# Kernel tuning notes

Measured on AMD Instinct MI355X. Metric: run time of the kernel, lower is better.

## Reference

```python
import jax, jax.numpy as jnp
import numpy as np

B, S, D = 2, 2048, 1024
N_HEADS = 16
HEAD_DIM = D // N_HEADS  # 64, even for RoPE
THETA = 10000.0


def rope_tables(seq, head_dim, dtype=jnp.float32):
    half = head_dim // 2
    freqs = 1.0 / (THETA ** (jnp.arange(half, dtype=jnp.float32) / half))
    angles = jnp.arange(seq, dtype=jnp.float32)[:, None] * freqs[None, :]  # [S, half]
    return jnp.cos(angles).astype(dtype), jnp.sin(angles).astype(dtype)


def apply_rope_interleaved(x, cos, sin):
    # x: [b, h, s, d]; even/odd interleaving
    x_even = x[..., 0::2]
    x_odd = x[..., 1::2]
    r_even = x_even * cos - x_odd * sin
    r_odd = x_even * sin + x_odd * cos
    # interleave back: stack on last axis then reshape
    out = jnp.stack([r_even, r_odd], axis=-1).reshape(x.shape)
    return out


def setup_inputs() -> dict:
    key = jax.random.key(0)
    ks = jax.random.split(key, 6)
    scale = 1.0 / np.sqrt(D)
    return {
        "x": jax.random.normal(ks[0], (B, S, D), dtype=jnp.float32),
        "Wq": jax.random.normal(ks[1], (D, D), dtype=jnp.float32) * scale,
        "Wk": jax.random.normal(ks[2], (D, D), dtype=jnp.float32) * scale,
        "Wv": jax.random.normal(ks[3], (D, D), dtype=jnp.float32) * scale,
        "Wo": jax.random.normal(ks[4], (D, D), dtype=jnp.float32) * scale,
        "bo": jnp.zeros((D,), dtype=jnp.float32),
    }


def reference(x, Wq, Wk, Wv, Wo, bo):
    b, s, _ = x.shape
    # QKV projections (no bias), split heads -> [b, h, s, hd]
    def proj(W):
        return jnp.einsum('bsd,de->bse', x, W).reshape(b, s, N_HEADS, HEAD_DIM).transpose(0, 2, 1, 3)
    q, k, v = proj(Wq), proj(Wk), proj(Wv)

    cos, sin = rope_tables(s, HEAD_DIM, x.dtype)  # [s, hd//2]
    q = apply_rope_interleaved(q, cos, sin)
    k = apply_rope_interleaved(k, cos, sin)

    scale = 1.0 / jnp.sqrt(jnp.asarray(HEAD_DIM, dtype=x.dtype))
    scores = jnp.einsum('bhqd,bhkd->bhqk', q, k) * scale  # [b, h, s, s]
    causal = jnp.tril(jnp.ones((s, s), dtype=bool))
    scores = jnp.where(causal[None, None], scores, jnp.asarray(-jnp.inf, dtype=scores.dtype))
    attn = jax.nn.softmax(scores, axis=-1)
    ctx = jnp.einsum('bhqk,bhkd->bhqd', attn, v)  # [b, h, s, hd]
    ctx = ctx.transpose(0, 2, 1, 3).reshape(b, s, N_HEADS * HEAD_DIM)
    return jnp.einsum('bsd,de->bse', ctx, Wo) + bo
```

## Files before the change

### kernel.cpp

```cpp
#include <hip/hip_runtime.h>
#include <hip/hip_bf16.h>
#include <math.h>

constexpr int Bb   = 2;
constexpr int S    = 2048;
constexpr int D    = 1024;
constexpr int H    = 16;
constexpr int Dh   = 64;
constexpr int HALF = 32;
constexpr int M    = Bb * S;
constexpr int K    = 1024;
constexpr int N    = 1024;

typedef __attribute__((ext_vector_type(8))) short short8;
typedef __attribute__((ext_vector_type(4))) float f32x4;

__device__ __forceinline__ unsigned short f2bf(float f) {
    unsigned int u = __float_as_uint(f);
    unsigned int r = (u + 0x7fffu + ((u >> 16) & 1u)) >> 16;
    return (unsigned short)r;
}

__device__ __forceinline__ void gl_lds16(const unsigned short* g, unsigned short* lds_base) {
    __builtin_amdgcn_global_load_lds(
        (const __attribute__((address_space(1))) unsigned int*)g,
        (__attribute__((address_space(3))) unsigned int*)lds_base, 16, 0, 0);
}

__global__ __launch_bounds__(256) void prep_kernel(
    const float* __restrict__ x,
    const float* W0, const float* W1, const float* W2, const float* W3,
    unsigned short* __restrict__ xb,
    unsigned short* T0, unsigned short* T1, unsigned short* T2, unsigned short* T3,
    float* __restrict__ cosT, float* __restrict__ sinT)
{
    __shared__ float tile[64][65];
    const int bid = blockIdx.x;
    const int tid = threadIdx.x;

    if (bid < 256) {
        int idx = bid * 256 + tid;
        int s = idx >> 5;
        int i = idx & 31;
        double freq = exp(-(double)i * (log(10000.0) / 32.0));
        double ang  = (double)s * freq;
        cosT[idx] = (float)cos(ang);
        sinT[idx] = (float)sin(ang);
    } else if (bid < 256 + 4096) {
        size_t i = (size_t)(bid - 256) * 256 + tid;
        float4 v = *(const float4*)(x + i * 4);
        ushort4 pk;
        pk.x = f2bf(v.x); pk.y = f2bf(v.y); pk.z = f2bf(v.z); pk.w = f2bf(v.w);
        *(ushort4*)(xb + i * 4) = pk;
    } else {
        int wb = bid - 4352;
        int z  = wb >> 8;
        int rem = wb & 255;
        const float* W = (z == 0) ? W0 : (z == 1) ? W1 : (z == 2) ? W2 : W3;
        unsigned short* T = (z == 0) ? T0 : (z == 1) ? T1 : (z == 2) ? T2 : T3;
        const int bk = (rem >> 4) * 64;
        const int bn = (rem & 15) * 64;
        const int lr = tid >> 4;
        const int lc = (tid & 15) * 4;

        #pragma unroll
        for (int i = 0; i < 4; ++i) {
            int r = lr + i * 16;
            float4 v = *(const float4*)(W + (size_t)(bk + r) * N + bn + lc);
            tile[r][lc + 0] = v.x; tile[r][lc + 1] = v.y;
            tile[r][lc + 2] = v.z; tile[r][lc + 3] = v.w;
        }
        __syncthreads();
        #pragma unroll
        for (int i = 0; i < 4; ++i) {
            int nr = lr + i * 16;
            ushort4 pk;
            pk.x = f2bf(tile[lc + 0][nr]);
            pk.y = f2bf(tile[lc + 1][nr]);
            pk.z = f2bf(tile[lc + 2][nr]);
            pk.w = f2bf(tile[lc + 3][nr]);
            *(ushort4*)(T + (size_t)(bn + nr) * K + bk + lc) = pk;
        }
    }
}

__global__ __launch_bounds__(512, 2) void gemm_qkv_kernel(
    const unsigned short* __restrict__ A,
    const unsigned short* __restrict__ BT,
    unsigned short* outQ, unsigned short* outK, unsigned short* outV,
    const float* __restrict__ cosT, const float* __restrict__ sinT)
{
    constexpr int NT   = 32;
    constexpr int BUFS = 256 * 32;
    __shared__ __align__(16) unsigned short As[4 * BUFS];
    __shared__ __align__(16) unsigned short Bs[4 * BUFS];

    const int tid  = threadIdx.x;
    const int wid  = tid >> 6;
    const int lane = tid & 63;
    const int col  = lane & 15;
    const int quad = lane >> 4;
    const int wr   = wid >> 2;
    const int wc   = wid & 3;

    const int mbase = blockIdx.y * 256;
    const int nbase = blockIdx.x * 256;

    const int srow = lane >> 2;
    const int sch  = lane & 3;
    const unsigned short *pA0, *pA1, *pB0, *pB1;
    unsigned short *dA0, *dA1, *dB0, *dB1;
    {
        int r0 = wid * 16 + srow;
        int r1 = 128 + wid * 16 + srow;
        pA0 = A  + (size_t)(mbase + r0) * K + ((sch + (r0 >> 1)) & 3) * 8;
        pA1 = A  + (size_t)(mbase + r1) * K + ((sch + (r1 >> 1)) & 3) * 8;
        pB0 = BT + (size_t)(nbase + r0) * K + ((sch + (r0 >> 1)) & 3) * 8;
        pB1 = BT + (size_t)(nbase + r1) * K + ((sch + (r1 >> 1)) & 3) * 8;
        dA0 = &As[(wid * 16) * 32];
        dA1 = &As[(128 + wid * 16) * 32];
        dB0 = &Bs[(wid * 16) * 32];
        dB1 = &Bs[(128 + wid * 16) * 32];
    }

    int aoff[8], boff[4];
    #pragma unroll
    for (int f = 0; f < 8; ++f) {
        int r = wr * 128 + f * 16 + col;
        aoff[f] = r * 32 + ((quad - (r >> 1)) & 3) * 8;
    }
    #pragma unroll
    for (int n = 0; n < 4; ++n) {
        int r = wc * 64 + n * 16 + col;
        boff[n] = r * 32 + ((quad - (r >> 1)) & 3) * 8;
    }

    f32x4 acc[8][4];
    #pragma unroll
    for (int f = 0; f < 8; ++f)
        #pragma unroll
        for (int n = 0; n < 4; ++n) acc[f][n] = (f32x4)0.f;

    auto stageA = [&](int slot) {
        gl_lds16(pA0, dA0 + slot * BUFS); pA0 += 32;
        gl_lds16(pA1, dA1 + slot * BUFS); pA1 += 32;
    };
    auto stageB = [&](int slot) {
        gl_lds16(pB0, dB0 + slot * BUFS); pB0 += 32;
        gl_lds16(pB1, dB1 + slot * BUFS); pB1 += 32;
    };

    stageA(0); stageB(0);
    stageA(1); stageB(1);
    stageA(2); stageB(2);
    asm volatile("s_waitcnt vmcnt(8)" ::: "memory");
    __builtin_amdgcn_s_barrier();
    __builtin_amdgcn_sched_barrier(0);

    #pragma unroll 1
    for (int t = 0; t < NT; ++t) {
        const unsigned short* Ab = &As[(t & 3) * BUFS];
        const unsigned short* Bc = &Bs[(t & 3) * BUFS];
        const int nslot = (t + 3) & 3;
        short8 af[4], bf[4];

        #pragma unroll
        for (int i = 0; i < 4; ++i) af[i] = *(const short8*)&Ab[aoff[i]];
        #pragma unroll
        for (int n = 0; n < 4; ++n) bf[n] = *(const short8*)&Bc[boff[n]];
        if (t < NT - 3) stageA(nslot);
        __builtin_amdgcn_sched_barrier(0);
        __builtin_amdgcn_s_barrier();
        asm volatile("s_waitcnt lgkmcnt(0)" ::: "memory");
        __builtin_amdgcn_s_setprio(1);
        #pragma unroll
        for (int i = 0; i < 4; ++i)
            #pragma unroll
            for (int n = 0; n < 4; ++n)
                acc[i][n] = __builtin_amdgcn_mfma_f32_16x16x32_bf16(af[i], bf[n], acc[i][n], 0, 0, 0);
        __builtin_amdgcn_s_setprio(0);
        __builtin_amdgcn_sched_barrier(0);
        __builtin_amdgcn_s_barrier();
        __builtin_amdgcn_sched_barrier(0);

        #pragma unroll
        for (int i = 0; i < 4; ++i) af[i] = *(const short8*)&Ab[aoff[4 + i]];
        if (t < NT - 3) stageB(nslot);
        __builtin_amdgcn_sched_barrier(0);
        __builtin_amdgcn_s_barrier();
        asm volatile("s_waitcnt lgkmcnt(0)" ::: "memory");
        __builtin_amdgcn_s_setprio(1);
        #pragma unroll
        for (int i = 0; i < 4; ++i)
            #pragma unroll
            for (int n = 0; n < 4; ++n)
                acc[4 + i][n] = __builtin_amdgcn_mfma_f32_16x16x32_bf16(af[i], bf[n], acc[4 + i][n], 0, 0, 0);
        __builtin_amdgcn_s_setprio(0);
        if (t < NT - 3)       { asm volatile("s_waitcnt vmcnt(8)" ::: "memory"); }
        else if (t == NT - 3) { asm volatile("s_waitcnt vmcnt(4)" ::: "memory"); }
        else if (t == NT - 2) { asm volatile("s_waitcnt vmcnt(0)" ::: "memory"); }
        __builtin_amdgcn_s_barrier();
        __builtin_amdgcn_sched_barrier(0);
    }

    const int z = nbase >> 10;
    if (z < 2) {
        unsigned short* o = z ? outK : outQ;
        #pragma unroll
        for (int n = 0; n < 4; ++n) {
            int nl = (nbase & 1023) + wc * 64 + n * 16 + col;
            int h = nl >> 6, dh0 = nl & 63, p = dh0 >> 1;
            bool even = !(dh0 & 1);
            #pragma unroll
            for (int f = 0; f < 8; ++f)
                #pragma unroll
                for (int reg = 0; reg < 4; ++reg) {
                    int m_g = mbase + wr * 128 + f * 16 + quad * 4 + reg;
                    int b = m_g >> 11, s = m_g & 2047;
                    float v = acc[f][n][reg];
                    float part = __shfl_xor(v, 1, 64);
                    float c = cosT[s * HALF + p], sn = sinT[s * HALF + p];
                    float r = even ? (v * c - part * sn) : (v * c + part * sn);
                    o[((size_t)(b * H + h) * S + s) * Dh + dh0] = f2bf(r);
                }
        }
    } else {
        #pragma unroll
        for (int n = 0; n < 4; ++n) {
            int nl = (nbase & 1023) + wc * 64 + n * 16 + col;
            int h = nl >> 6, dh0 = nl & 63;
            #pragma unroll
            for (int f = 0; f < 8; ++f) {
                int m0 = mbase + wr * 128 + f * 16 + quad * 4;
                int b = m0 >> 11, s = m0 & 2047;
                ushort4 pk;
                pk.x = f2bf(acc[f][n][0]);
                pk.y = f2bf(acc[f][n][1]);
                pk.z = f2bf(acc[f][n][2]);
                pk.w = f2bf(acc[f][n][3]);
                *(ushort4*)&outV[((size_t)(b * H + h) * Dh + dh0) * S + s] = pk;
            }
        }
    }
}

__global__ __launch_bounds__(256) void gemm_out_kernel(
    const unsigned short* __restrict__ A,
    const unsigned short* __restrict__ BT,
    float* __restrict__ outO, const float* __restrict__ bias)
{
    constexpr int BK   = 64;
    constexpr int ABUF = 64 * BK;
    constexpr int BBUF = 64 * BK;
    __shared__ __align__(16) unsigned short As[2 * ABUF];
    __shared__ __align__(16) unsigned short Bs[2 * BBUF];

    const int tid  = threadIdx.x;
    const int wave = tid >> 6;
    const int lane = tid & 63;
    const int col  = lane & 15;
    const int quad = lane >> 4;
    const int wy   = wave >> 1;
    const int wx   = wave & 1;

    const int mbase = blockIdx.y * 64;
    const int nbase = blockIdx.x * 64;

    const int srow8 = lane >> 3;
    const int sch8  = lane & 7;

    const unsigned short *pA[2], *pB[2];
    unsigned short *dA[2], *dB[2];
    #pragma unroll
    for (int w = 0; w < 2; ++w) {
        int base = wave * 16 + w * 8;
        int tr = base + srow8;
        pA[w] = A  + (size_t)(mbase + tr) * K + ((sch8 + (tr >> 1)) & 7) * 8;
        pB[w] = BT + (size_t)(nbase + tr) * K + ((sch8 + (tr >> 1)) & 7) * 8;
        dA[w] = &As[base * BK];
        dB[w] = &Bs[base * BK];
    }

    int aoff[2][2], boff[2][2];
    #pragma unroll
    for (int ks = 0; ks < 2; ++ks) {
        #pragma unroll
        for (int mi = 0; mi < 2; ++mi) {
            int r = wy * 32 + mi * 16 + col;
            aoff[ks][mi] = r * BK + (((ks * 4 + quad) - (r >> 1)) & 7) * 8;
        }
        #pragma unroll
        for (int ni = 0; ni < 2; ++ni) {
            int r = wx * 32 + ni * 16 + col;
            boff[ks][ni] = r * BK + (((ks * 4 + quad) - (r >> 1)) & 7) * 8;
        }
    }

    f32x4 acc[2][2];
    #pragma unroll
    for (int mi = 0; mi < 2; ++mi)
        #pragma unroll
        for (int ni = 0; ni < 2; ++ni) acc[mi][ni] = (f32x4)0.f;

    auto stage = [&](int buf) {
        #pragma unroll
        for (int w = 0; w < 2; ++w) { gl_lds16(pA[w], dA[w] + buf * ABUF); pA[w] += BK; }
        #pragma unroll
        for (int w = 0; w < 2; ++w) { gl_lds16(pB[w], dB[w] + buf * BBUF); pB[w] += BK; }
    };
    auto compute = [&](int buf) {
        const unsigned short* Ac = &As[buf * ABUF];
        const unsigned short* Bc = &Bs[buf * BBUF];
        #pragma unroll
        for (int ks = 0; ks < 2; ++ks) {
            short8 af[2], bfr[2];
            #pragma unroll
            for (int mi = 0; mi < 2; ++mi) af[mi] = *(const short8*)&Ac[aoff[ks][mi]];
            #pragma unroll
            for (int ni = 0; ni < 2; ++ni) bfr[ni] = *(const short8*)&Bc[boff[ks][ni]];
            #pragma unroll
            for (int mi = 0; mi < 2; ++mi)
                #pragma unroll
                for (int ni = 0; ni < 2; ++ni)
                    acc[mi][ni] = __builtin_amdgcn_mfma_f32_16x16x32_bf16(af[mi], bfr[ni], acc[mi][ni], 0, 0, 0);
        }
    };

    stage(0);
    #pragma unroll 1
    for (int kk = 0; kk < 16; kk += 2) {
        __syncthreads();
        if (kk + 1 < 16) stage(1);
        compute(0);
        __syncthreads();
        if (kk + 2 < 16) stage(0);
        compute(1);
    }

    #pragma unroll
    for (int ni = 0; ni < 2; ++ni) {
        int n_g = nbase + wx * 32 + ni * 16 + col;
        float bv = bias[n_g];
        #pragma unroll
        for (int mi = 0; mi < 2; ++mi)
            #pragma unroll
            for (int reg = 0; reg < 4; ++reg) {
                int m_g = mbase + wy * 32 + mi * 16 + quad * 4 + reg;
                outO[(size_t)m_g * N + n_g] = acc[mi][ni][reg] + bv;
            }
    }
}

__global__ __launch_bounds__(256) void attn_mfma_kernel(
    const unsigned short* __restrict__ q, const unsigned short* __restrict__ k,
    const unsigned short* __restrict__ vt, unsigned short* __restrict__ ctx)
{
    constexpr int TSZ = 64 * 64;
    __shared__ __align__(16) unsigned short Ks[4 * TSZ];
    __shared__ __align__(16) unsigned short Vs[4 * TSZ];
    __shared__ __align__(16) unsigned short Ps[4][16 * 72];

    const int tid  = threadIdx.x;
    const int wave = tid >> 6;
    const int lane = tid & 63;
    const int col  = lane & 15;
    const int quad = lane >> 4;
    const int l8   = lane >> 3, cp = lane & 7;

    const int bh = blockIdx.y;
    const unsigned short* qb = q  + (size_t)bh * S * Dh;
    const unsigned short* kb = k  + (size_t)bh * S * Dh;
    const unsigned short* vb = vt + (size_t)bh * Dh * S;
    const int b = bh >> 4, h = bh & 15;

    unsigned short* dk0 = &Ks[(wave * 16 + 0) * 64];
    unsigned short* dk1 = &Ks[(wave * 16 + 8) * 64];
    unsigned short* dv0 = &Vs[(wave * 16 + 0) * 64];
    unsigned short* dv1 = &Vs[(wave * 16 + 8) * 64];

    int foff[2][4];
    #pragma unroll
    for (int ks = 0; ks < 2; ++ks)
        #pragma unroll
        for (int nt = 0; nt < 4; ++nt) {
            int r = nt * 16 + col;
            foff[ks][nt] = r * 64 + (((ks * 4 + quad) - r) & 7) * 8;
        }
    int poffW[4][4];
    #pragma unroll
    for (int nt = 0; nt < 4; ++nt)
        #pragma unroll
        for (int reg = 0; reg < 4; ++reg)
            poffW[nt][reg] = (quad * 4 + reg) * 72 + nt * 16 + col;
    const int poffR0 = col * 72 + quad * 8;

    for (int phase = 0; phase < 2; ++phase) {
        const int qt  = phase ? (31 - (int)blockIdx.x) : (int)blockIdx.x;
        const int wr0 = qt * 64 + wave * 16;

        const unsigned short *pk0, *pk1, *pv0, *pv1, *ok0, *ok1, *ov0, *ov1;
        {
            int r0 = wave * 16 + l8, r1 = r0 + 8;
            pk0 = kb + (size_t)r0 * Dh + ((cp + r0) & 7) * 8;
            pk1 = kb + (size_t)r1 * Dh + ((cp + r1) & 7) * 8;
            pv0 = vb + (size_t)r0 * S + ((cp + r0) & 7) * 8;
            pv1 = vb + (size_t)r1 * S + ((cp + r1) & 7) * 8;
            ok0 = pk0 + 64 * Dh; ok1 = pk1 + 64 * Dh;
            ov0 = pv0 + 64;      ov1 = pv1 + 64;
        }

        __syncthreads();
        gl_lds16(pk0, dk0); gl_lds16(pk1, dk1);
        gl_lds16(pv0, dv0); gl_lds16(pv1, dv1);
        if (qt >= 1) {
            gl_lds16(ok0, dk0 + TSZ); gl_lds16(ok1, dk1 + TSZ);
            gl_lds16(ov0, dv0 + TSZ); gl_lds16(ov1, dv1 + TSZ);
        }
        pk0 += 128 * Dh; pk1 += 128 * Dh; pv0 += 128; pv1 += 128;
        ok0 += 128 * Dh; ok1 += 128 * Dh; ov0 += 128; ov1 += 128;

        short8 qfrag[2];
        #pragma unroll
        for (int ks = 0; ks < 2; ++ks)
            qfrag[ks] = *(const short8*)(qb + (size_t)(wr0 + col) * Dh + ks * 32 + quad * 8);

        f32x4 O[4];
        float lacc[4];
        #pragma unroll
        for (int nt = 0; nt < 4; ++nt) O[nt] = (f32x4)0.f;
        #pragma unroll
        for (int r = 0; r < 4; ++r) lacc[r] = 0.f;

        auto subtile = [&](const unsigned short* Kc, const unsigned short* Vc, int t) {
            f32x4 sacc[4];
            #pragma unroll
            for (int nt = 0; nt < 4; ++nt) sacc[nt] = (f32x4)0.f;
            #pragma unroll
            for (int ks = 0; ks < 2; ++ks)
                #pragma unroll
                for (int nt = 0; nt < 4; ++nt) {
                    short8 kf = *(const short8*)&Kc[foff[ks][nt]];
                    sacc[nt] = __builtin_amdgcn_mfma_f32_16x16x32_bf16(qfrag[ks], kf, sacc[nt], 0, 0, 0);
                }
            float pb[4][4];
            #pragma unroll
            for (int nt = 0; nt < 4; ++nt) {
                int key_l = nt * 16 + col;
                #pragma unroll
                for (int reg = 0; reg < 4; ++reg) {
                    float e = __expf(fmaf(sacc[nt][reg], 0.125f, -8.0f));
                    if (t == qt && key_l > wave * 16 + quad * 4 + reg) e = 0.f;
                    pb[nt][reg] = e;
                }
            }
            #pragma unroll
            for (int reg = 0; reg < 4; ++reg)
                lacc[reg] += (pb[0][reg] + pb[1][reg]) + (pb[2][reg] + pb[3][reg]);
            #pragma unroll
            for (int nt = 0; nt < 4; ++nt)
                #pragma unroll
                for (int reg = 0; reg < 4; ++reg)
                    Ps[wave][poffW[nt][reg]] = f2bf(pb[nt][reg]);
            #pragma unroll
            for (int ks = 0; ks < 2; ++ks) {
                short8 pf = *(const short8*)&Ps[wave][poffR0 + ks * 32];
                #pragma unroll
                for (int nt = 0; nt < 4; ++nt) {
                    short8 vf = *(const short8*)&Vc[foff[ks][nt]];
                    O[nt] = __builtin_amdgcn_mfma_f32_16x16x32_bf16(pf, vf, O[nt], 0, 0, 0);
                }
            }
        };

        const int nint = (qt >> 1) + 1;
        for (int i = 0; i < nint; ++i) {
            __syncthreads();
            const int ta = 2 * i;
            if (ta + 2 <= qt) {
                const int nb = ((i + 1) & 1) * 2 * TSZ;
                gl_lds16(pk0, dk0 + nb); gl_lds16(pk1, dk1 + nb);
                gl_lds16(pv0, dv0 + nb); gl_lds16(pv1, dv1 + nb);
                if (ta + 3 <= qt) {
                    gl_lds16(ok0, dk0 + nb + TSZ); gl_lds16(ok1, dk1 + nb + TSZ);
                    gl_lds16(ov0, dv0 + nb + TSZ); gl_lds16(ov1, dv1 + nb + TSZ);
                }
                pk0 += 128 * Dh; pk1 += 128 * Dh; pv0 += 128; pv1 += 128;
                ok0 += 128 * Dh; ok1 += 128 * Dh; ov0 += 128; ov1 += 128;
            }
            const unsigned short* Kc = &Ks[(i & 1) * 2 * TSZ];
            const unsigned short* Vc = &Vs[(i & 1) * 2 * TSZ];
            subtile(Kc, Vc, ta);
            if (ta + 1 <= qt) subtile(Kc + TSZ, Vc + TSZ, ta + 1);
        }

        #pragma unroll
        for (int reg = 0; reg < 4; ++reg) {
            float s = lacc[reg];
            #pragma unroll
            for (int off = 1; off <= 8; off <<= 1)
                s += __shfl_xor(s, off, 64);
            lacc[reg] = s;
        }

        #pragma unroll
        for (int reg = 0; reg < 4; ++reg) {
            float inv = 1.0f / lacc[reg];
            int rg = wr0 + quad * 4 + reg;
            unsigned short* dst = ctx + ((size_t)b * S + rg) * 1024 + h * 64 + col;
            #pragma unroll
            for (int nt = 0; nt < 4; ++nt)
                dst[nt * 16] = f2bf(O[nt][reg] * inv);
        }
    }
}

extern "C" void kernel_launch(void* const* d_in, const int* in_sizes, int n_in,
                              void* d_out, int out_size, void* d_ws, size_t ws_size,
                              hipStream_t stream) {
    const float* x  = (const float*)d_in[0];
    const float* Wq = (const float*)d_in[1];
    const float* Wk = (const float*)d_in[2];
    const float* Wv = (const float*)d_in[3];
    const float* Wo = (const float*)d_in[4];
    const float* bo = (const float*)d_in[5];
    float* out = (float*)d_out;

    const size_t MK  = (size_t)M * K;
    const size_t NK  = (size_t)N * K;
    const size_t QKV = (size_t)Bb * H * S * Dh;

    unsigned short* xb   = (unsigned short*)d_ws;
    unsigned short* WqT  = xb  + MK;
    unsigned short* WkT  = WqT + NK;
    unsigned short* WvT  = WkT + NK;
    unsigned short* WoT  = WvT + NK;
    unsigned short* qbuf = WoT + NK;
    unsigned short* kbuf = qbuf + QKV;
    unsigned short* vtb  = kbuf + QKV;
    unsigned short* ctxb = vtb  + QKV;
    float* cosT = (float*)(ctxb + QKV);
    float* sinT = cosT + (size_t)S * HALF;

    prep_kernel<<<5376, 256, 0, stream>>>(x, Wq, Wk, Wv, Wo,
                                          xb, WqT, WkT, WvT, WoT, cosT, sinT);

    gemm_qkv_kernel<<<dim3(12, 16), 512, 0, stream>>>(
        xb, WqT, qbuf, kbuf, vtb, cosT, sinT);

    attn_mfma_kernel<<<dim3(16, Bb * H), 256, 0, stream>>>(qbuf, kbuf, vtb, ctxb);

    gemm_out_kernel<<<dim3(16, 64), 256, 0, stream>>>(ctxb, WoT, out, bo);
}
```

Measured before the change: 189.2 us.

## Shrink attention LDS staging to 64-key tiles with XOR-swizzled P buffer

The attention kernel's K/V staging goes from double-buffered 128-key chunks to double-buffered 64-key tiles, cutting the shared-memory footprint roughly in half so more blocks can be resident per CU. The padded P scratch (stride 72) becomes an XOR-swizzled stride-64 layout to avoid bank conflicts while saving LDS. The exponential is now a direct exp2 with the scale and offset folded in by log2(e). In exchange there are twice as many barriers per key range and less prefetch distance.

Result: no change. 189.3 us (+0.1%).

```diff
diff --git a/kernel.cpp b/kernel.cpp
--- a/kernel.cpp
+++ b/kernel.cpp
@@ -356,9 +356,9 @@
     const unsigned short* __restrict__ vt, unsigned short* __restrict__ ctx)
 {
     constexpr int TSZ = 64 * 64;
-    __shared__ __align__(16) unsigned short Ks[4 * TSZ];
-    __shared__ __align__(16) unsigned short Vs[4 * TSZ];
-    __shared__ __align__(16) unsigned short Ps[4][16 * 72];
+    __shared__ __align__(16) unsigned short Ks[2 * TSZ];
+    __shared__ __align__(16) unsigned short Vs[2 * TSZ];
+    __shared__ __align__(16) unsigned short Ps[4][16 * 64];
 
     const int tid  = threadIdx.x;
     const int wave = tid >> 6;
@@ -390,34 +390,36 @@
     #pragma unroll
     for (int nt = 0; nt < 4; ++nt)
         #pragma unroll
-        for (int reg = 0; reg < 4; ++reg)
-            poffW[nt][reg] = (quad * 4 + reg) * 72 + nt * 16 + col;
-    const int poffR0 = col * 72 + quad * 8;
+        for (int reg = 0; reg < 4; ++reg) {
+            int row = quad * 4 + reg;
+            poffW[nt][reg] = row * 64 + (((nt * 2 + (col >> 3)) ^ (row & 7)) << 3) + (col & 7);
+        }
+    int poffR[2];
+    #pragma unroll
+    for (int ks = 0; ks < 2; ++ks)
+        poffR[ks] = col * 64 + (((ks * 4 + quad) ^ (col & 7)) << 3);
 
     for (int phase = 0; phase < 2; ++phase) {
         const int qt  = phase ? (31 - (int)blockIdx.x) : (int)blockIdx.x;
         const int wr0 = qt * 64 + wave * 16;
 
-        const unsigned short *pk0, *pk1, *pv0, *pv1, *ok0, *ok1, *ov0, *ov1;
+        const unsigned short *pk0, *pk1, *pv0, *pv1;
         {
             int r0 = wave * 16 + l8, r1 = r0 + 8;
             pk0 = kb + (size_t)r0 * Dh + ((cp + r0) & 7) * 8;
             pk1 = kb + (size_t)r1 * Dh + ((cp + r1) & 7) * 8;
             pv0 = vb + (size_t)r0 * S + ((cp + r0) & 7) * 8;
             pv1 = vb + (size_t)r1 * S + ((cp + r1) & 7) * 8;
-            ok0 = pk0 + 64 * Dh; ok1 = pk1 + 64 * Dh;
-            ov0 = pv0 + 64;      ov1 = pv1 + 64;
-        }
+        }
+
+        auto stageKV = [&](int buf) {
+            gl_lds16(pk0, dk0 + buf * TSZ); gl_lds16(pk1, dk1 + buf * TSZ);
+            gl_lds16(pv0, dv0 + buf * TSZ); gl_lds16(pv1, dv1 + buf * TSZ);
+            pk0 += 64 * Dh; pk1 += 64 * Dh; pv0 += 64; pv1 += 64;
+        };
 
         __syncthreads();
-        gl_lds16(pk0, dk0); gl_lds16(pk1, dk1);
-        gl_lds16(pv0, dv0); gl_lds16(pv1, dv1);
-        if (qt >= 1) {
-            gl_lds16(ok0, dk0 + TSZ); gl_lds16(ok1, dk1 + TSZ);
-            gl_lds16(ov0, dv0 + TSZ); gl_lds16(ov1, dv1 + TSZ);
-        }
-        pk0 += 128 * Dh; pk1 += 128 * Dh; pv0 += 128; pv1 += 128;
-        ok0 += 128 * Dh; ok1 += 128 * Dh; ov0 += 128; ov1 += 128;
+        stageKV(0);
 
         short8 qfrag[2];
         #pragma unroll
@@ -448,7 +450,8 @@
                 int key_l = nt * 16 + col;
                 #pragma unroll
                 for (int reg = 0; reg < 4; ++reg) {
-                    float e = __expf(fmaf(sacc[nt][reg], 0.125f, -8.0f));
+                    float e = __builtin_amdgcn_exp2f(
+                        fmaf(sacc[nt][reg], 0.18033688011112042f, -11.541560327111707f));
                     if (t == qt && key_l > wave * 16 + quad * 4 + reg) e = 0.f;
                     pb[nt][reg] = e;
                 }
@@ -463,7 +466,7 @@
                     Ps[wave][poffW[nt][reg]] = f2bf(pb[nt][reg]);
             #pragma unroll
             for (int ks = 0; ks < 2; ++ks) {
-                short8 pf = *(const short8*)&Ps[wave][poffR0 + ks * 32];
+                short8 pf = *(const short8*)&Ps[wave][poffR[ks]];
                 #pragma unroll
                 for (int nt = 0; nt < 4; ++nt) {
                     short8 vf = *(const short8*)&Vc[foff[ks][nt]];
@@ -472,25 +475,10 @@
             }
         };
 
-        const int nint = (qt >> 1) + 1;
-        for (int i = 0; i < nint; ++i) {
+        for (int i = 0; i <= qt; ++i) {
             __syncthreads();
-            const int ta = 2 * i;
-            if (ta + 2 <= qt) {
-                const int nb = ((i + 1) & 1) * 2 * TSZ;
-                gl_lds16(pk0, dk0 + nb); gl_lds16(pk1, dk1 + nb);
-                gl_lds16(pv0, dv0 + nb); gl_lds16(pv1, dv1 + nb);
-                if (ta + 3 <= qt) {
-                    gl_lds16(ok0, dk0 + nb + TSZ); gl_lds16(ok1, dk1 + nb + TSZ);
-                    gl_lds16(ov0, dv0 + nb + TSZ); gl_lds16(ov1, dv1 + nb + TSZ);
-                }
-                pk0 += 128 * Dh; pk1 += 128 * Dh; pv0 += 128; pv1 += 128;
-                ok0 += 128 * Dh; ok1 += 128 * Dh; ov0 += 128; ov1 += 128;
-            }
-            const unsigned short* Kc = &Ks[(i & 1) * 2 * TSZ];
-            const unsigned short* Vc = &Vs[(i & 1) * 2 * TSZ];
-            subtile(Kc, Vc, ta);
-            if (ta + 1 <= qt) subtile(Kc + TSZ, Vc + TSZ, ta + 1);
+            if (i < qt) stageKV((i + 1) & 1);
+            subtile(&Ks[(i & 1) * TSZ], &Vs[(i & 1) * TSZ], i);
         }
 
         #pragma unroll
```
